# Performance work log

Hardware: AMD Instinct MI355X
Metric: run time of the kernel (lower is better)

## Reference

```python
import jax, jax.numpy as jnp
import numpy as np


def setup_inputs() -> dict:
    key = jax.random.key(0)
    kq, kk, kv = jax.random.split(key, 3)
    B, S, D = 32, 2048, 128
    q = jax.random.normal(kq, (B, S, D), dtype=jnp.float32)
    k = jax.random.normal(kk, (B, S, D), dtype=jnp.float32)
    v = jax.random.normal(kv, (B, S, D), dtype=jnp.float32)
    return {"q": q, "k": k, "v": v}


def reference(q, k, v):
    # scaled = exp(QK^T / sqrt(d_k)); attn = scaled / sum(scaled) ; out = attn @ V
    # (softmax computed via raw exp/sum, matching the original module; no mask,
    #  dropout is identity in eval mode)
    d_k = q.shape[2]
    scale = 1.0 / jnp.sqrt(jnp.asarray(d_k, dtype=q.dtype))
    scores = jnp.einsum("bqd,bkd->bqk", q, k) * scale  # [B, S, S]
    e = jnp.exp(scores)
    attn = e / jnp.sum(e, axis=-1, keepdims=True)
    return jnp.einsum("bqk,bkd->bqd", attn, v)
```

## Files before the change

kernel.cpp:

```cpp
#include <hip/hip_runtime.h>
#include <hip/hip_bf16.h>
#include <stdint.h>

typedef __attribute__((ext_vector_type(8))) __bf16 bf16x8;
typedef __attribute__((ext_vector_type(4))) float  f32x4;
typedef __attribute__((ext_vector_type(2))) unsigned int u32x2;

#define S_  2048
#define D_  128
#define QB  128
#define KB  32
#define NT  (S_/KB)
#define VPANEL 1056
#define VBUF   (8*VPANEL)

__device__ __forceinline__ __bf16 f2bf(float f){ return (__bf16)f; }

__device__ __forceinline__ bf16x8 pack8(float4 a, float4 b){
  bf16x8 r;
  r[0]=f2bf(a.x); r[1]=f2bf(a.y); r[2]=f2bf(a.z); r[3]=f2bf(a.w);
  r[4]=f2bf(b.x); r[5]=f2bf(b.y); r[6]=f2bf(b.z); r[7]=f2bf(b.w);
  return r;
}

__global__ __launch_bounds__(256, 2)
void attn_fwd(const float* __restrict__ Q, const float* __restrict__ K,
              const float* __restrict__ V, float* __restrict__ O) {
  __shared__ __align__(128) __bf16 k_lds[2][KB][136];
  __shared__ __align__(128) unsigned char v_raw[2][VBUF];

  const int t   = threadIdx.x;
  const int w   = t >> 6;
  const int l   = t & 63;
  const int l16 = l & 15;
  const int lg  = l >> 4;

  const int f  = blockIdx.x;
  const int b  = ((f & 7) << 2) | ((f >> 3) & 3);
  const int bq = f >> 5;

  const float* Qb = Q + (size_t)b * (S_*D_);
  const float* Kb = K + (size_t)b * (S_*D_);
  const float* Vb = V + (size_t)b * (S_*D_);
  float*       Ob = O + (size_t)b * (S_*D_);

  const int q0 = bq*QB + w*32;
  const float qscale = 0.08838834764831845f * 1.4426950408889634f;

  bf16x8 qf[2][4];
  #pragma unroll
  for (int qt=0; qt<2; ++qt){
    const float* qr = Qb + (size_t)(q0 + qt*16 + l16) * D_;
    #pragma unroll
    for (int ds=0; ds<4; ++ds){
      const float4* p = (const float4*)(qr + ds*32 + lg*8);
      float4 a = p[0], c = p[1];
      a.x*=qscale; a.y*=qscale; a.z*=qscale; a.w*=qscale;
      c.x*=qscale; c.y*=qscale; c.z*=qscale; c.w*=qscale;
      qf[qt][ds] = pack8(a, c);
    }
  }

  f32x4 acc[2][8];
  #pragma unroll
  for (int qt=0; qt<2; ++qt)
    #pragma unroll
    for (int dt=0; dt<8; ++dt)
      acc[qt][dt] = (f32x4){0.f,0.f,0.f,0.f};
  float den0 = 0.f, den1 = 0.f;

  const int sr  = t >> 3;
  const int sdt = t & 7;
  const int par = sdt & 1;
  const float* Kst = Kb + (size_t)sr * D_ + sdt*16;
  const float* Vst = Vb + (size_t)sr * D_ + sdt*16;

  float4 kst0,kst1,kst2,kst3, vst0,vst1,vst2,vst3;

  #define LOADT(IT) do { \
    const float4* kp_ = (const float4*)(Kst + (size_t)(IT)*KB*D_); \
    const float4* vp_ = (const float4*)(Vst + (size_t)(IT)*KB*D_); \
    kst0=kp_[0]; kst1=kp_[1]; kst2=kp_[2]; kst3=kp_[3]; \
    vst0=vp_[0]; vst1=vp_[1]; vst2=vp_[2]; vst3=vp_[3]; \
  } while(0)

  #define WRITET(BUF) do { \
    *(bf16x8*)&k_lds[BUF][sr][sdt*16    ] = pack8(kst0,kst1); \
    *(bf16x8*)&k_lds[BUF][sr][sdt*16 + 8] = pack8(kst2,kst3); \
    unsigned char* vb_ = &v_raw[BUF][sdt*VPANEL + sr*32]; \
    *(bf16x8*)(vb_ + (par<<4))        = pack8(vst0,vst1); \
    *(bf16x8*)(vb_ + ((par^1)<<4))    = pack8(vst2,vst3); \
  } while(0)

  const unsigned vbase   = (unsigned)(uintptr_t)&v_raw[0][0];
  const unsigned troff_e = (unsigned)(lg*128 + (l16>>2)*32 + ((l16&3)*8));
  const unsigned troff_o = (unsigned)(lg*128 + (l16>>2)*32 + (((l16&3)*8) ^ 16));

  u32x2 vlo[8], vhi[8];
  bf16x8 pf[2];

  #define QK_BLOCK(CUR, SVAR) do { \
    __builtin_amdgcn_s_setprio(1); \
    _Pragma("unroll") \
    for (int ct=0; ct<2; ++ct){ \
      bf16x8 kf[4]; \
      _Pragma("unroll") \
      for (int ds=0; ds<4; ++ds) \
        kf[ds] = *(const bf16x8*)&k_lds[CUR][ct*16 + l16][ds*32 + lg*8]; \
      _Pragma("unroll") \
      for (int qt=0; qt<2; ++qt){ \
        f32x4 sv = (f32x4){0.f,0.f,0.f,0.f}; \
        _Pragma("unroll") \
        for (int ds=0; ds<4; ++ds) \
          sv = __builtin_amdgcn_mfma_f32_16x16x32_bf16(kf[ds], qf[qt][ds], sv, 0,0,0); \
        SVAR[qt][ct] = sv; \
      } \
    } \
    __builtin_amdgcn_s_setprio(0); \
  } while(0)

  #define PV_BLOCK() do { \
    __builtin_amdgcn_s_setprio(1); \
    _Pragma("unroll") \
    for (int dt=0; dt<8; ++dt){ \
      union { bf16x8 v; u32x2 u[2]; } uu; \
      uu.u[0] = vlo[dt]; uu.u[1] = vhi[dt]; \
      acc[0][dt] = __builtin_amdgcn_mfma_f32_16x16x32_bf16(uu.v, pf[0], acc[0][dt], 0,0,0); \
      acc[1][dt] = __builtin_amdgcn_mfma_f32_16x16x32_bf16(uu.v, pf[1], acc[1][dt], 0,0,0); \
    } \
    __builtin_amdgcn_s_setprio(0); \
  } while(0)

  #define EXP_BLOCK(SVAR) do { \
    _Pragma("unroll") \
    for (int qt=0; qt<2; ++qt){ \
      float dsum = 0.f; \
      _Pragma("unroll") \
      for (int ct=0; ct<2; ++ct){ \
        _Pragma("unroll") \
        for (int r=0; r<4; ++r){ \
          float e = __builtin_amdgcn_exp2f(SVAR[qt][ct][r]); \
          dsum += e; \
          pf[qt][ct*4+r] = f2bf(e); \
        } \
      } \
      if (qt==0) den0 += dsum; else den1 += dsum; \
    } \
  } while(0)

  #define TR_ISSUE(CUR) do { \
    const unsigned vb_e = vbase + (unsigned)((CUR)*VBUF) + troff_e; \
    const unsigned vb_o = vbase + (unsigned)((CUR)*VBUF) + troff_o; \
    _Pragma("unroll") \
    for (int dt=0; dt<8; ++dt){ \
      const unsigned a = ((dt & 1) ? vb_o : vb_e) + (unsigned)(dt*VPANEL); \
      asm volatile("ds_read_b64_tr_b16 %0, %2\n\t" \
                   "ds_read_b64_tr_b16 %1, %2 offset:512" \
                   : "=&v"(vlo[dt]), "=&v"(vhi[dt]) \
                   : "v"(a)); \
    } \
  } while(0)

  #define FENCE() do { \
    asm volatile("s_waitcnt lgkmcnt(0)" ::: "memory"); \
    __builtin_amdgcn_sched_barrier(0); \
    __syncthreads(); \
  } while(0)

  LOADT(0); WRITET(0); LOADT(1);
  __syncthreads();

  {
    TR_ISSUE(0);
    WRITET(1);
    LOADT(2);
    f32x4 s0[2][2];
    QK_BLOCK(0, s0);
    EXP_BLOCK(s0);
    FENCE();
  }

  for (int it = 1; it < NT; ++it){
    const int cur = it & 1;

    PV_BLOCK();
    TR_ISSUE(cur);
    if (it+1 < NT) WRITET(cur^1);
    if (it+2 < NT) LOADT(it+2);

    f32x4 s[2][2];
    QK_BLOCK(cur, s);
    EXP_BLOCK(s);
    FENCE();
  }

  PV_BLOCK();

  #pragma unroll
  for (int qt=0; qt<2; ++qt){
    float dsum = (qt==0) ? den0 : den1;
    dsum += __shfl_xor(dsum, 16);
    dsum += __shfl_xor(dsum, 32);
    const float inv = 1.0f / dsum;
    float* orow = Ob + (size_t)(q0 + qt*16 + l16) * D_ + lg*4;
    #pragma unroll
    for (int dt=0; dt<8; ++dt){
      f32x4 a4 = acc[qt][dt];
      float4 o4;
      o4.x = a4[0]*inv; o4.y = a4[1]*inv; o4.z = a4[2]*inv; o4.w = a4[3]*inv;
      *(float4*)(orow + dt*16) = o4;
    }
  }
}

extern "C" void kernel_launch(void* const* d_in, const int* in_sizes, int n_in,
                              void* d_out, int out_size, void* d_ws, size_t ws_size,
                              hipStream_t stream) {
  const float* q = (const float*)d_in[0];
  const float* k = (const float*)d_in[1];
  const float* v = (const float*)d_in[2];
  float* o = (float*)d_out;
  attn_fwd<<<dim3(512), dim3(256), 0, stream>>>(q, k, v, o);
}
```

Baseline: 90.28 us.

## Triple-buffer K/V LDS tiles and prefetch K fragments one tile ahead

Moves from double to triple buffering of the K and V tiles in shared memory. The global-load pipeline now runs three tiles ahead, and the K MFMA fragments for the next tile are read from LDS into registers during the current iteration, before the exp stage. The goal is to hide LDS read latency ahead of the QK MFMAs and to give global loads more slack. In exchange, LDS use per block grows by half, and the extra prefetched fragments raise register pressure, which may hurt the 2-blocks-per-CU occupancy target.

```diff
diff --git a/kernel.cpp b/kernel.cpp
--- a/kernel.cpp
+++ b/kernel.cpp
@@ -26,8 +26,8 @@
 __global__ __launch_bounds__(256, 2)
 void attn_fwd(const float* __restrict__ Q, const float* __restrict__ K,
               const float* __restrict__ V, float* __restrict__ O) {
-  __shared__ __align__(128) __bf16 k_lds[2][KB][136];
-  __shared__ __align__(128) unsigned char v_raw[2][VBUF];
+  __shared__ __align__(128) __bf16 k_lds[3][KB][136];
+  __shared__ __align__(128) unsigned char v_raw[3][VBUF];
 
   const int t   = threadIdx.x;
   const int w   = t >> 6;
@@ -98,21 +98,26 @@
 
   u32x2 vlo[8], vhi[8];
   bf16x8 pf[2];
-
-  #define QK_BLOCK(CUR, SVAR) do { \
-    __builtin_amdgcn_s_setprio(1); \
-    _Pragma("unroll") \
-    for (int ct=0; ct<2; ++ct){ \
-      bf16x8 kf[4]; \
+  bf16x8 kfp[2][4];
+
+  #define KF_PREFETCH(BUF) do { \
+    _Pragma("unroll") \
+    for (int ct=0; ct<2; ++ct) \
       _Pragma("unroll") \
       for (int ds=0; ds<4; ++ds) \
-        kf[ds] = *(const bf16x8*)&k_lds[CUR][ct*16 + l16][ds*32 + lg*8]; \
+        kfp[ct][ds] = *(const bf16x8*)&k_lds[BUF][ct*16 + l16][ds*32 + lg*8]; \
+  } while(0)
+
+  #define QK_REG(SVAR) do { \
+    __builtin_amdgcn_s_setprio(1); \
+    _Pragma("unroll") \
+    for (int ct=0; ct<2; ++ct){ \
       _Pragma("unroll") \
       for (int qt=0; qt<2; ++qt){ \
         f32x4 sv = (f32x4){0.f,0.f,0.f,0.f}; \
         _Pragma("unroll") \
         for (int ds=0; ds<4; ++ds) \
-          sv = __builtin_amdgcn_mfma_f32_16x16x32_bf16(kf[ds], qf[qt][ds], sv, 0,0,0); \
+          sv = __builtin_amdgcn_mfma_f32_16x16x32_bf16(kfp[ct][ds], qf[qt][ds], sv, 0,0,0); \
         SVAR[qt][ct] = sv; \
       } \
     } \
@@ -148,9 +153,9 @@
     } \
   } while(0)
 
-  #define TR_ISSUE(CUR) do { \
-    const unsigned vb_e = vbase + (unsigned)((CUR)*VBUF) + troff_e; \
-    const unsigned vb_o = vbase + (unsigned)((CUR)*VBUF) + troff_o; \
+  #define TR_ISSUE(BUF) do { \
+    const unsigned vb_e = vbase + (unsigned)((BUF)*VBUF) + troff_e; \
+    const unsigned vb_o = vbase + (unsigned)((BUF)*VBUF) + troff_o; \
     _Pragma("unroll") \
     for (int dt=0; dt<8; ++dt){ \
       const unsigned a = ((dt & 1) ? vb_o : vb_e) + (unsigned)(dt*VPANEL); \
@@ -167,31 +172,38 @@
     __syncthreads(); \
   } while(0)
 
-  LOADT(0); WRITET(0); LOADT(1);
+  LOADT(0); WRITET(0);
+  LOADT(1); WRITET(1);
+  LOADT(2);
   __syncthreads();
+
+  int cur = 0, nx1 = 1, nx2 = 2;
 
   {
     TR_ISSUE(0);
-    WRITET(1);
-    LOADT(2);
+    WRITET(2);
+    LOADT(3);
+    KF_PREFETCH(0);
     f32x4 s0[2][2];
-    QK_BLOCK(0, s0);
+    QK_REG(s0);
+    KF_PREFETCH(1);
     EXP_BLOCK(s0);
     FENCE();
+    int tmp = cur; cur = nx1; nx1 = nx2; nx2 = tmp;
   }
 
   for (int it = 1; it < NT; ++it){
-    const int cur = it & 1;
-
     PV_BLOCK();
     TR_ISSUE(cur);
-    if (it+1 < NT) WRITET(cur^1);
-    if (it+2 < NT) LOADT(it+2);
+    if (it+2 < NT) WRITET(nx2);
+    if (it+3 < NT) LOADT(it+3);
 
     f32x4 s[2][2];
-    QK_BLOCK(cur, s);
+    QK_REG(s);
+    if (it+1 < NT) KF_PREFETCH(nx1);
     EXP_BLOCK(s);
     FENCE();
+    int tmp = cur; cur = nx1; nx1 = nx2; nx2 = tmp;
   }
 
   PV_BLOCK();
```

New measurement: 91.14 us. About the same (+1.0%).

## Switch attention MFMAs from 16x16x32 to 32x32x16 bf16 tiles

Applied to the files above, without the earlier changes.

Replaces the 16x16x32 bf16 MFMA tiling with 32x32x16 MFMAs for both the QK^T and PV products. Each wave now handles its 32 query rows as one 32x32 tile, so it needs fewer LDS K-fragment loads and fewer MFMA issues per tile. The V transpose reads, the exp/denominator layout and the output store mapping are reworked to match. The larger MFMA has longer latency and changes register layout and LDS access patterns, which could affect bank conflicts and overlap.

```diff
diff --git a/kernel.cpp b/kernel.cpp
--- a/kernel.cpp
+++ b/kernel.cpp
@@ -2,9 +2,10 @@
 #include <hip/hip_bf16.h>
 #include <stdint.h>
 
-typedef __attribute__((ext_vector_type(8))) __bf16 bf16x8;
-typedef __attribute__((ext_vector_type(4))) float  f32x4;
-typedef __attribute__((ext_vector_type(2))) unsigned int u32x2;
+typedef __attribute__((ext_vector_type(8)))  __bf16 bf16x8;
+typedef __attribute__((ext_vector_type(4)))  float  f32x4;
+typedef __attribute__((ext_vector_type(16))) float  f32x16;
+typedef __attribute__((ext_vector_type(2)))  unsigned int u32x2;
 
 #define S_  2048
 #define D_  128
@@ -32,8 +33,10 @@
   const int t   = threadIdx.x;
   const int w   = t >> 6;
   const int l   = t & 63;
-  const int l16 = l & 15;
-  const int lg  = l >> 4;
+  const int l31 = l & 31;
+  const int hi  = l >> 5;
+  const int p16 = l & 15;
+  const int pg  = (l >> 4) & 1;
 
   const int f  = blockIdx.x;
   const int b  = ((f & 7) << 2) | ((f >> 3) & 3);
@@ -47,27 +50,26 @@
   const int q0 = bq*QB + w*32;
   const float qscale = 0.08838834764831845f * 1.4426950408889634f;
 
-  bf16x8 qf[2][4];
-  #pragma unroll
-  for (int qt=0; qt<2; ++qt){
-    const float* qr = Qb + (size_t)(q0 + qt*16 + l16) * D_;
-    #pragma unroll
-    for (int ds=0; ds<4; ++ds){
-      const float4* p = (const float4*)(qr + ds*32 + lg*8);
+  bf16x8 qf[8];
+  {
+    const float* qr = Qb + (size_t)(q0 + l31) * D_;
+    #pragma unroll
+    for (int ds=0; ds<8; ++ds){
+      const float4* p = (const float4*)(qr + ds*16 + hi*8);
       float4 a = p[0], c = p[1];
       a.x*=qscale; a.y*=qscale; a.z*=qscale; a.w*=qscale;
       c.x*=qscale; c.y*=qscale; c.z*=qscale; c.w*=qscale;
-      qf[qt][ds] = pack8(a, c);
+      qf[ds] = pack8(a, c);
     }
   }
 
-  f32x4 acc[2][8];
+  f32x16 acc[4];
   #pragma unroll
-  for (int qt=0; qt<2; ++qt)
-    #pragma unroll
-    for (int dt=0; dt<8; ++dt)
-      acc[qt][dt] = (f32x4){0.f,0.f,0.f,0.f};
-  float den0 = 0.f, den1 = 0.f;
+  for (int tt=0; tt<4; ++tt)
+    #pragma unroll
+    for (int c=0; c<16; ++c)
+      acc[tt][c] = 0.f;
+  float den = 0.f;
 
   const int sr  = t >> 3;
   const int sdt = t & 7;
@@ -92,73 +94,58 @@
     *(bf16x8*)(vb_ + ((par^1)<<4))    = pack8(vst2,vst3); \
   } while(0)
 
-  const unsigned vbase   = (unsigned)(uintptr_t)&v_raw[0][0];
-  const unsigned troff_e = (unsigned)(lg*128 + (l16>>2)*32 + ((l16&3)*8));
-  const unsigned troff_o = (unsigned)(lg*128 + (l16>>2)*32 + (((l16&3)*8) ^ 16));
-
-  u32x2 vlo[8], vhi[8];
+  const unsigned vbase = (unsigned)(uintptr_t)&v_raw[0][0];
+  const unsigned tro   = (unsigned)(pg*VPANEL + hi*128 + (p16>>2)*32 + (((p16&3)*8) ^ (pg*16)));
+
+  u32x2 vq[4][4];
   bf16x8 pf[2];
+
+  #define TR_ISSUE(CUR) do { \
+    _Pragma("unroll") \
+    for (int tt=0; tt<4; ++tt){ \
+      const unsigned a = vbase + (unsigned)((CUR)*VBUF) + (unsigned)(tt*2*VPANEL) + tro; \
+      asm volatile("ds_read_b64_tr_b16 %0, %4\n\t" \
+                   "ds_read_b64_tr_b16 %1, %4 offset:256\n\t" \
+                   "ds_read_b64_tr_b16 %2, %4 offset:512\n\t" \
+                   "ds_read_b64_tr_b16 %3, %4 offset:768" \
+                   : "=&v"(vq[tt][0]), "=&v"(vq[tt][1]), \
+                     "=&v"(vq[tt][2]), "=&v"(vq[tt][3]) \
+                   : "v"(a)); \
+    } \
+  } while(0)
 
   #define QK_BLOCK(CUR, SVAR) do { \
     __builtin_amdgcn_s_setprio(1); \
     _Pragma("unroll") \
-    for (int ct=0; ct<2; ++ct){ \
-      bf16x8 kf[4]; \
-      _Pragma("unroll") \
-      for (int ds=0; ds<4; ++ds) \
-        kf[ds] = *(const bf16x8*)&k_lds[CUR][ct*16 + l16][ds*32 + lg*8]; \
-      _Pragma("unroll") \
-      for (int qt=0; qt<2; ++qt){ \
-        f32x4 sv = (f32x4){0.f,0.f,0.f,0.f}; \
-        _Pragma("unroll") \
-        for (int ds=0; ds<4; ++ds) \
-          sv = __builtin_amdgcn_mfma_f32_16x16x32_bf16(kf[ds], qf[qt][ds], sv, 0,0,0); \
-        SVAR[qt][ct] = sv; \
-      } \
+    for (int ds=0; ds<8; ++ds){ \
+      bf16x8 kf = *(const bf16x8*)&k_lds[CUR][l31][ds*16 + hi*8]; \
+      SVAR = __builtin_amdgcn_mfma_f32_32x32x16_bf16(kf, qf[ds], SVAR, 0,0,0); \
     } \
     __builtin_amdgcn_s_setprio(0); \
+  } while(0)
+
+  #define EXP_BLOCK(SVAR) do { \
+    _Pragma("unroll") \
+    for (int r=0; r<16; ++r){ \
+      float e = __builtin_amdgcn_exp2f(SVAR[r]); \
+      den += e; \
+      pf[r>>3][r&7] = f2bf(e); \
+    } \
   } while(0)
 
   #define PV_BLOCK() do { \
     __builtin_amdgcn_s_setprio(1); \
     _Pragma("unroll") \
-    for (int dt=0; dt<8; ++dt){ \
-      union { bf16x8 v; u32x2 u[2]; } uu; \
-      uu.u[0] = vlo[dt]; uu.u[1] = vhi[dt]; \
-      acc[0][dt] = __builtin_amdgcn_mfma_f32_16x16x32_bf16(uu.v, pf[0], acc[0][dt], 0,0,0); \
-      acc[1][dt] = __builtin_amdgcn_mfma_f32_16x16x32_bf16(uu.v, pf[1], acc[1][dt], 0,0,0); \
+    for (int tt=0; tt<4; ++tt){ \
+      _Pragma("unroll") \
+      for (int s=0; s<2; ++s){ \
+        union { bf16x8 v; u32x2 u[2]; } uu; \
+        uu.u[0] = vq[tt][s*2]; \
+        uu.u[1] = vq[tt][s*2+1]; \
+        acc[tt] = __builtin_amdgcn_mfma_f32_32x32x16_bf16(uu.v, pf[s], acc[tt], 0,0,0); \
+      } \
     } \
     __builtin_amdgcn_s_setprio(0); \
-  } while(0)
-
-  #define EXP_BLOCK(SVAR) do { \
-    _Pragma("unroll") \
-    for (int qt=0; qt<2; ++qt){ \
-      float dsum = 0.f; \
-      _Pragma("unroll") \
-      for (int ct=0; ct<2; ++ct){ \
-        _Pragma("unroll") \
-        for (int r=0; r<4; ++r){ \
-          float e = __builtin_amdgcn_exp2f(SVAR[qt][ct][r]); \
-          dsum += e; \
-          pf[qt][ct*4+r] = f2bf(e); \
-        } \
-      } \
-      if (qt==0) den0 += dsum; else den1 += dsum; \
-    } \
-  } while(0)
-
-  #define TR_ISSUE(CUR) do { \
-    const unsigned vb_e = vbase + (unsigned)((CUR)*VBUF) + troff_e; \
-    const unsigned vb_o = vbase + (unsigned)((CUR)*VBUF) + troff_o; \
-    _Pragma("unroll") \
-    for (int dt=0; dt<8; ++dt){ \
-      const unsigned a = ((dt & 1) ? vb_o : vb_e) + (unsigned)(dt*VPANEL); \
-      asm volatile("ds_read_b64_tr_b16 %0, %2\n\t" \
-                   "ds_read_b64_tr_b16 %1, %2 offset:512" \
-                   : "=&v"(vlo[dt]), "=&v"(vhi[dt]) \
-                   : "v"(a)); \
-    } \
   } while(0)
 
   #define FENCE() do { \
@@ -174,9 +161,11 @@
     TR_ISSUE(0);
     WRITET(1);
     LOADT(2);
-    f32x4 s0[2][2];
-    QK_BLOCK(0, s0);
-    EXP_BLOCK(s0);
+    f32x16 sv;
+    #pragma unroll
+    for (int c=0; c<16; ++c) sv[c] = 0.f;
+    QK_BLOCK(0, sv);
+    EXP_BLOCK(sv);
     FENCE();
   }
 
@@ -188,27 +177,29 @@
     if (it+1 < NT) WRITET(cur^1);
     if (it+2 < NT) LOADT(it+2);
 
-    f32x4 s[2][2];
-    QK_BLOCK(cur, s);
-    EXP_BLOCK(s);
+    f32x16 sv;
+    #pragma unroll
+    for (int c=0; c<16; ++c) sv[c] = 0.f;
+    QK_BLOCK(cur, sv);
+    EXP_BLOCK(sv);
     FENCE();
   }
 
   PV_BLOCK();
 
-  #pragma unroll
-  for (int qt=0; qt<2; ++qt){
-    float dsum = (qt==0) ? den0 : den1;
-    dsum += __shfl_xor(dsum, 16);
-    dsum += __shfl_xor(dsum, 32);
+  {
+    float dsum = den + __shfl_xor(den, 32);
     const float inv = 1.0f / dsum;
-    float* orow = Ob + (size_t)(q0 + qt*16 + l16) * D_ + lg*4;
-    #pragma unroll
-    for (int dt=0; dt<8; ++dt){
-      f32x4 a4 = acc[qt][dt];
-      float4 o4;
-      o4.x = a4[0]*inv; o4.y = a4[1]*inv; o4.z = a4[2]*inv; o4.w = a4[3]*inv;
-      *(float4*)(orow + dt*16) = o4;
+    float* orow = Ob + (size_t)(q0 + l31) * D_;
+    #pragma unroll
+    for (int tt=0; tt<4; ++tt){
+      #pragma unroll
+      for (int rq=0; rq<4; ++rq){
+        float4 o4;
+        o4.x = acc[tt][4*rq+0]*inv; o4.y = acc[tt][4*rq+1]*inv;
+        o4.z = acc[tt][4*rq+2]*inv; o4.w = acc[tt][4*rq+3]*inv;
+        *(float4*)(orow + tt*32 + 8*rq + 4*hi) = o4;
+      }
     }
   }
 }
```

Result: slower. 98.45 us (+9.1%).
